# Kernel tuning notes

Measured on AMD Instinct MI355X. Metric: run time of the kernel, lower is better.

The kernel has to match this reference:

```python
import jax, jax.numpy as jnp
import numpy as np

IN_F = 64
EDGE_F = 64
B, N = 2, 512


def setup_inputs() -> dict:
    key = jax.random.key(0)
    ks = jax.random.split(key, 10)
    h = jax.random.normal(ks[0], (B, N, IN_F), dtype=jnp.float32)
    edge = jax.random.normal(ks[1], (B, N, N, EDGE_F), dtype=jnp.float32)
    adj = (jax.random.uniform(ks[2], (B, N, N)) < 0.5).astype(jnp.float32)
    lin_in = 2 * IN_F + EDGE_F
    s_lin = 1.0 / np.sqrt(lin_in)
    s_gru = 1.0 / np.sqrt(EDGE_F)
    W_lin = jax.random.uniform(ks[3], (EDGE_F, lin_in), minval=-s_lin, maxval=s_lin)
    b_lin = jax.random.uniform(ks[4], (EDGE_F,), minval=-s_lin, maxval=s_lin)
    w_ih = jax.random.uniform(ks[5], (3 * EDGE_F, EDGE_F), minval=-s_gru, maxval=s_gru)
    w_hh = jax.random.uniform(ks[6], (3 * EDGE_F, EDGE_F), minval=-s_gru, maxval=s_gru)
    b_ih = jax.random.uniform(ks[7], (3 * EDGE_F,), minval=-s_gru, maxval=s_gru)
    b_hh = jax.random.uniform(ks[8], (3 * EDGE_F,), minval=-s_gru, maxval=s_gru)
    return {"h": h, "edge": edge, "adj": adj, "W_lin": W_lin, "b_lin": b_lin,
            "w_ih": w_ih, "w_hh": w_hh, "b_ih": b_ih, "b_hh": b_hh}


def reference(h, edge, adj, W_lin, b_lin, w_ih, w_hh, b_ih, b_hh):
    F_ = h.shape[-1]
    E = edge.shape[-1]
    # Split the concat-linear: cat = [h1, edge, h2] where h1[b,i,j]=h[b,j], h2[b,i,j]=h[b,i].
    W1 = W_lin[:, :F_]            # cols acting on h1
    We = W_lin[:, F_:F_ + E]      # cols acting on edge
    W2 = W_lin[:, F_ + E:]        # cols acting on h2
    t1 = jnp.einsum('bjf,ef->bje', h, W1)[:, None, :, :]   # broadcast over i
    t2 = jnp.einsum('bif,ef->bie', h, W2)[:, :, None, :]   # broadcast over j
    te = jnp.einsum('bije,fe->bijf', edge, We)
    m = (t1 + te + t2 + b_lin) * adj[..., None]            # [b,N,N,E]
    # GRUCell: input = m, hidden = edge
    gi = jnp.einsum('bije,ge->bijg', m, w_ih) + b_ih        # [b,N,N,3E]
    gh = jnp.einsum('bije,ge->bijg', edge, w_hh) + b_hh
    i_r, i_z, i_n = jnp.split(gi, 3, axis=-1)
    h_r, h_z, h_n = jnp.split(gh, 3, axis=-1)
    r = jax.nn.sigmoid(i_r + h_r)
    z = jax.nn.sigmoid(i_z + h_z)
    n = jnp.tanh(i_n + r * h_n)
    new_h = (1.0 - z) * n + z * edge
    return jax.nn.silu(new_h)
```

## Files before the change

### kernel.cpp

```cpp
#include <hip/hip_runtime.h>
#include <hip/hip_bf16.h>

#define B_ 2
#define N_ 512
#define E_ 64
#define G_ 192
#define LIN_IN_ 192

typedef __attribute__((ext_vector_type(8))) short bf16x8;
typedef __attribute__((ext_vector_type(4))) float f32x4;

__device__ __forceinline__ unsigned short f2bf(float x) {
  unsigned u = __float_as_uint(x);
  unsigned r = (u + 0x7FFFu + ((u >> 16) & 1u)) >> 16;
  return (unsigned short)r;
}
__device__ __forceinline__ float sigm(float x) {
  return __builtin_amdgcn_rcpf(1.f + __expf(-x));
}
__device__ __forceinline__ float tanh_f(float x) {
  float e = __expf(-2.f * fabsf(x));
  return copysignf((1.f - e) * __builtin_amdgcn_rcpf(1.f + e), x);
}
__device__ __forceinline__ bf16x8 pack8(const float* t) {
  union { bf16x8 v; __hip_bfloat16 h[8]; } u;
#pragma unroll
  for (int k = 0; k < 8; ++k) u.h[k] = __float2bfloat16(t[k]);
  return u.v;
}

__global__ __launch_bounds__(64) void prep1(const float* __restrict__ Wlin,
                                            const float* __restrict__ blin,
                                            const float* __restrict__ wih,
                                            const float* __restrict__ whh,
                                            unsigned short* __restrict__ Bt,
                                            float* __restrict__ V1,
                                            float* __restrict__ V2,
                                            float* __restrict__ ub) {
  int g = blockIdx.x;
  int f = threadIdx.x;
  if (g < G_) {
    const float* wr = wih + g * 64;
    float aw = 0.f, a1 = 0.f, a2 = 0.f;
#pragma unroll
    for (int e = 0; e < 64; ++e) {
      float wv = wr[e];
      a1 += wv * Wlin[e * LIN_IN_ + f];
      aw += wv * Wlin[e * LIN_IN_ + 64 + f];
      a2 += wv * Wlin[e * LIN_IN_ + 128 + f];
    }
    Bt[g * 64 + f] = f2bf(aw);
    V1[g * 64 + f] = a1;
    V2[g * 64 + f] = a2;
    if (f == 0) {
      float s = 0.f;
      for (int e = 0; e < 64; ++e) s += wr[e] * blin[e];
      ub[g] = s;
    }
  } else {
    int gh = g - G_;
    Bt[g * 64 + f] = f2bf(whh[gh * 64 + f]);
  }
}

__global__ __launch_bounds__(192) void prep2(const float* __restrict__ h,
                                             const float* __restrict__ V1,
                                             const float* __restrict__ V2,
                                             const float* __restrict__ ub,
                                             float* __restrict__ u1,
                                             float* __restrict__ u2p) {
  int row = blockIdx.x;
  int g = threadIdx.x;
  const float* hr = h + (size_t)row * 64;
  float a1 = 0.f, a2 = 0.f;
#pragma unroll
  for (int f = 0; f < 64; ++f) {
    float hv = hr[f];
    a1 += V1[g * 64 + f] * hv;
    a2 += V2[g * 64 + f] * hv;
  }
  u1[(size_t)row * G_ + g] = a1;
  u2p[(size_t)row * G_ + g] = a2 + ub[g];
}

__global__ __launch_bounds__(256) void fusedT14(const float* __restrict__ edge,
                                                const float* __restrict__ adj,
                                                const unsigned short* __restrict__ BtW,
                                                const float* __restrict__ u1,
                                                const float* __restrict__ u2p,
                                                const float* __restrict__ bih,
                                                const float* __restrict__ bhh,
                                                float* __restrict__ out) {
  __shared__ uint4 Bs4[3072];
  char* Bc = (char*)Bs4;
  int tid = threadIdx.x;

  int lane = tid & 63, wave = tid >> 6;
  unsigned pbase = blockIdx.x * 256u + wave * 32u;
  int b = pbase >> 18;
  int iN = (pbase >> 9) & 511;
  int lr = lane & 15, lg = lane >> 4;

  float4 raw[2][4];
  float adjraw[2];
#pragma unroll
  for (int np = 0; np < 2; ++np) {
    const float* er = edge + (size_t)(pbase + np * 16 + lr) * 64 + lg * 8;
    raw[np][0] = *(const float4*)er;
    raw[np][1] = *(const float4*)(er + 4);
    raw[np][2] = *(const float4*)(er + 32);
    raw[np][3] = *(const float4*)(er + 36);
    adjraw[np] = adj[pbase + np * 16 + lr];
  }

  const uint4* src = (const uint4*)BtW;
#pragma unroll
  for (int it = 0; it < 12; ++it) {
    int c = tid + it * 256;
    int row = c >> 3;
    *(uint4*)(Bc + row * 128 + (((c & 7) * 16) ^ ((row & 7) << 4))) = src[c];
  }
  __syncthreads();

  int addrE = (lr + 16 * (lg >> 1)) << 2;
  int addrO = addrE + 128;

  const float* u2r = u2p + ((size_t)(b * N_ + iN)) * G_;

#pragma unroll
  for (int t = 0; t < 2; ++t) {
    unsigned ptile = pbase + (unsigned)t * 128u;
    int j0w = (int)(ptile & 511);

    bf16x8 efrag[2][2];
    float adjv[2];
#pragma unroll
    for (int np = 0; np < 2; ++np) {
#pragma unroll
      for (int s = 0; s < 2; ++s) {
        float tmp[8];
        *(float4*)tmp = raw[np][s * 2];
        *(float4*)(tmp + 4) = raw[np][s * 2 + 1];
        efrag[np][s] = pack8(tmp);
      }
      adjv[np] = adjraw[np];
    }

    if (t == 0) {
      unsigned pnext = pbase + 128u;
#pragma unroll
      for (int np = 0; np < 2; ++np) {
        const float* er = edge + (size_t)(pnext + np * 16 + lr) * 64 + lg * 8;
        raw[np][0] = *(const float4*)er;
        raw[np][1] = *(const float4*)(er + 4);
        raw[np][2] = *(const float4*)(er + 32);
        raw[np][3] = *(const float4*)(er + 36);
        adjraw[np] = adj[pnext + np * 16 + lr];
      }
    }

    const float* u1b = u1 + ((size_t)(b * N_ + j0w)) * G_;

    f32x4 yo[2][4];

#pragma unroll
    for (int mg = 0; mg < 4; ++mg) {
      int e0 = mg * 16 + lg * 4;

      f32x4 u1v[2][3];
#pragma unroll
      for (int np = 0; np < 2; ++np) {
        const float* u1r = u1b + (size_t)(np * 16 + lr) * G_;
        u1v[np][0] = *(const f32x4*)(u1r + e0);
        u1v[np][1] = *(const f32x4*)(u1r + 64 + e0);
        u1v[np][2] = *(const f32x4*)(u1r + 128 + e0);
      }

      f32x4 acc[2][6];
      f32x4 zero = {0.f, 0.f, 0.f, 0.f};
#pragma unroll
      for (int np = 0; np < 2; ++np)
#pragma unroll
        for (int w = 0; w < 6; ++w) acc[np][w] = zero;

      const int tiles[6] = {mg, mg + 4, mg + 8, mg + 12, mg + 16, mg + 20};
#pragma unroll
      for (int s = 0; s < 2; ++s) {
        bf16x8 wf[6];
#pragma unroll
        for (int w = 0; w < 6; ++w) {
          int R = tiles[w] * 16 + lr;
          wf[w] = *(const bf16x8*)(Bc + R * 128 +
                                   ((s * 64 + lg * 16) ^ ((R & 7) << 4)));
        }
#pragma unroll
        for (int np = 0; np < 2; ++np)
#pragma unroll
          for (int w = 0; w < 6; ++w)
            acc[np][w] = __builtin_amdgcn_mfma_f32_16x16x32_bf16(
                wf[w], efrag[np][s], acc[np][w], 0, 0, 0);
      }

      f32x4 u2v0 = *(const f32x4*)(u2r + e0);
      f32x4 u2v1 = *(const f32x4*)(u2r + 64 + e0);
      f32x4 u2v2 = *(const f32x4*)(u2r + 128 + e0);
      f32x4 bc0 = *(const f32x4*)(bih + e0) + *(const f32x4*)(bhh + e0);
      f32x4 bc1 = *(const f32x4*)(bih + 64 + e0) + *(const f32x4*)(bhh + 64 + e0);
      f32x4 bi2 = *(const f32x4*)(bih + 128 + e0);
      f32x4 bh2 = *(const f32x4*)(bhh + 128 + e0);

#pragma unroll
      for (int np = 0; np < 2; ++np) {
        union { bf16x8 v; int d[4]; } ef;
        ef.v = efrag[np][mg >> 1];
        int addr = (mg & 1) ? addrO : addrE;
        int r0 = __builtin_amdgcn_ds_bpermute(addr, ef.d[0]);
        int r1 = __builtin_amdgcn_ds_bpermute(addr, ef.d[1]);
        int r2 = __builtin_amdgcn_ds_bpermute(addr, ef.d[2]);
        int r3 = __builtin_amdgcn_ds_bpermute(addr, ef.d[3]);
        bool hi = (lg & 1);
        unsigned w0 = (unsigned)(hi ? r2 : r0);
        unsigned w1 = (unsigned)(hi ? r3 : r1);
        float eva[4];
        eva[0] = __uint_as_float(w0 << 16);
        eva[1] = __uint_as_float(w0 & 0xffff0000u);
        eva[2] = __uint_as_float(w1 << 16);
        eva[3] = __uint_as_float(w1 & 0xffff0000u);

        float a = adjv[np];
        f32x4 yv;
#pragma unroll
        for (int reg = 0; reg < 4; ++reg) {
          float s1 = a * (acc[np][0][reg] + u1v[np][0][reg] + u2v0[reg]) +
                     bc0[reg] + acc[np][3][reg];
          float s2 = a * (acc[np][1][reg] + u1v[np][1][reg] + u2v1[reg]) +
                     bc1[reg] + acc[np][4][reg];
          float gin = a * (acc[np][2][reg] + u1v[np][2][reg] + u2v2[reg]) +
                      bi2[reg];
          float ghn = acc[np][5][reg] + bh2[reg];
          float r = sigm(s1);
          float z = sigm(s2);
          float tt = gin + r * ghn;
          float n = 2.f * sigm(2.f * tt) - 1.f;
          float y = n + z * (eva[reg] - n);
          yv[reg] = y * sigm(y);
        }
        yo[np][mg] = yv;
      }
    }

#pragma unroll
    for (int np = 0; np < 2; ++np) {
      size_t P = ptile + np * 16 + lr;
      float* op = out + P * 64 + lg * 4;
#pragma unroll
      for (int mg = 0; mg < 4; ++mg)
        *(f32x4*)(op + mg * 16) = yo[np][mg];
    }
  }
}

__global__ __launch_bounds__(64) void mkernelF(const float* __restrict__ edge,
                                               const float* __restrict__ adj,
                                               const float* __restrict__ Wlin,
                                               const float* __restrict__ blin,
                                               const float* __restrict__ h,
                                               float* __restrict__ mout) {
  size_t p = (size_t)blockIdx.x * 64 + threadIdx.x;
  int b = (int)(p >> 18), i = (int)((p >> 9) & 511), j = (int)(p & 511);
  float ed[E_], hj[E_], hi[E_];
  const float4* ep = (const float4*)(edge + p * E_);
  const float4* hjp = (const float4*)(h + ((size_t)(b * N_ + j)) * E_);
  const float4* hip = (const float4*)(h + ((size_t)(b * N_ + i)) * E_);
#pragma unroll
  for (int k = 0; k < E_ / 4; ++k) {
    float4 v = ep[k];
    ed[4 * k] = v.x; ed[4 * k + 1] = v.y; ed[4 * k + 2] = v.z; ed[4 * k + 3] = v.w;
    float4 a = hjp[k];
    hj[4 * k] = a.x; hj[4 * k + 1] = a.y; hj[4 * k + 2] = a.z; hj[4 * k + 3] = a.w;
    float4 u = hip[k];
    hi[4 * k] = u.x; hi[4 * k + 1] = u.y; hi[4 * k + 2] = u.z; hi[4 * k + 3] = u.w;
  }
  float av = adj[p];
  float* mo = mout + p * E_;
  for (int e = 0; e < E_; ++e) {
    const float* w = Wlin + e * LIN_IN_;
    float acc = blin[e];
#pragma unroll
    for (int k = 0; k < E_; ++k)
      acc += hj[k] * w[k] + ed[k] * w[64 + k] + hi[k] * w[128 + k];
    mo[e] = av * acc;
  }
}
__global__ __launch_bounds__(64) void gkernelF(const float* __restrict__ edge,
                                               const float* mbuf,
                                               const float* __restrict__ wih,
                                               const float* __restrict__ whh,
                                               const float* __restrict__ bih,
                                               const float* __restrict__ bhh,
                                               float* out) {
  size_t p = (size_t)blockIdx.x * 64 + threadIdx.x;
  float ed[E_], m[E_];
  const float4* ep = (const float4*)(edge + p * E_);
  const float4* mp = (const float4*)(mbuf + p * E_);
#pragma unroll
  for (int k = 0; k < E_ / 4; ++k) {
    float4 v = ep[k];
    ed[4 * k] = v.x; ed[4 * k + 1] = v.y; ed[4 * k + 2] = v.z; ed[4 * k + 3] = v.w;
    float4 u = mp[k];
    m[4 * k] = u.x; m[4 * k + 1] = u.y; m[4 * k + 2] = u.z; m[4 * k + 3] = u.w;
  }
  float* op = out + p * E_;
  for (int e = 0; e < E_; ++e) {
    const float* wr = wih + e * 64;
    const float* wz = wih + (64 + e) * 64;
    const float* wn = wih + (128 + e) * 64;
    const float* vr = whh + e * 64;
    const float* vz = whh + (64 + e) * 64;
    const float* vn = whh + (128 + e) * 64;
    float ir = bih[e], iz = bih[64 + e], inn = bih[128 + e];
    float hr = bhh[e], hz = bhh[64 + e], hn = bhh[128 + e];
#pragma unroll
    for (int k = 0; k < E_; ++k) {
      float mk = m[k], ek = ed[k];
      ir += mk * wr[k]; iz += mk * wz[k]; inn += mk * wn[k];
      hr += ek * vr[k]; hz += ek * vz[k]; hn += ek * vn[k];
    }
    float r = sigm(ir + hr);
    float z = sigm(iz + hz);
    float nv = tanh_f(inn + r * hn);
    float nh = (1.f - z) * nv + z * ed[e];
    op[e] = nh * sigm(nh);
  }
}

extern "C" void kernel_launch(void* const* d_in, const int* in_sizes, int n_in,
                              void* d_out, int out_size, void* d_ws, size_t ws_size,
                              hipStream_t stream) {
  const float* h    = (const float*)d_in[0];
  const float* edge = (const float*)d_in[1];
  const float* adj  = (const float*)d_in[2];
  const float* Wlin = (const float*)d_in[3];
  const float* blin = (const float*)d_in[4];
  const float* wih  = (const float*)d_in[5];
  const float* whh  = (const float*)d_in[6];
  const float* bih  = (const float*)d_in[7];
  const float* bhh  = (const float*)d_in[8];
  float* out = (float*)d_out;

  const size_t OFF_V1 = 49152, OFF_V2 = 98304, OFF_UB = 147456,
               OFF_U1 = 148480, OFF_U2 = 148480 + 786432;
  const size_t WS_NEEDED = OFF_U2 + 786432;
  if (ws_size >= WS_NEEDED) {
    char* w = (char*)d_ws;
    unsigned short* Bt = (unsigned short*)w;
    float* V1 = (float*)(w + OFF_V1);
    float* V2 = (float*)(w + OFF_V2);
    float* ub = (float*)(w + OFF_UB);
    float* u1 = (float*)(w + OFF_U1);
    float* u2p = (float*)(w + OFF_U2);
    prep1<<<384, 64, 0, stream>>>(Wlin, blin, wih, whh, Bt, V1, V2, ub);
    prep2<<<B_ * N_, 192, 0, stream>>>(h, V1, V2, ub, u1, u2p);
    fusedT14<<<2048, 256, 0, stream>>>(edge, adj, Bt, u1, u2p, bih, bhh, out);
  } else {
    size_t npairs = (size_t)B_ * N_ * N_;
    int blocks = (int)(npairs / 64);
    mkernelF<<<blocks, 64, 0, stream>>>(edge, adj, Wlin, blin, h, out);
    gkernelF<<<blocks, 64, 0, stream>>>(edge, out, wih, whh, bih, bhh, out);
  }
}
```

Before: 123.8 us.

## Make fused GRU kernel persistent with cross-group edge prefetch

Converts the fused MFMA GRU kernel from 2048 one-shot blocks to a persistent grid of 768 blocks that loop over groups with a stride. The weight tile is staged into LDS once per block instead of once per group, and the next group's edge/adj loads are issued while the current second tile is computed, so global latency overlaps across group boundaries. The tile math is factored into a helper. Fewer resident blocks may reduce latency hiding, and 2048 groups over 768 blocks leaves some blocks doing three groups and others two, so the load is uneven.

```diff
diff --git a/kernel.cpp b/kernel.cpp
--- a/kernel.cpp
+++ b/kernel.cpp
@@ -6,6 +6,8 @@
 #define E_ 64
 #define G_ 192
 #define LIN_IN_ 192
+#define NGROUP_ 2048u
+#define GSTRIDE_ 768u
 
 typedef __attribute__((ext_vector_type(8))) short bf16x8;
 typedef __attribute__((ext_vector_type(4))) float f32x4;
@@ -83,7 +85,112 @@
   u2p[(size_t)row * G_ + g] = a2 + ub[g];
 }
 
-__global__ __launch_bounds__(256) void fusedT14(const float* __restrict__ edge,
+__device__ __forceinline__ void compute_tile(
+    unsigned ptile, int b, const bf16x8 efrag[2][2], const float adjv[2],
+    const char* Bc, const float* __restrict__ u1, const float* __restrict__ u2r,
+    const float* __restrict__ bih, const float* __restrict__ bhh,
+    float* __restrict__ out, int lr, int lg, int addrE, int addrO) {
+  int j0w = (int)(ptile & 511);
+  const float* u1b = u1 + ((size_t)(b * N_ + j0w)) * G_;
+  f32x4 yo[2][4];
+
+#pragma unroll
+  for (int mg = 0; mg < 4; ++mg) {
+    int e0 = mg * 16 + lg * 4;
+
+    f32x4 u1v[2][3];
+#pragma unroll
+    for (int np = 0; np < 2; ++np) {
+      const float* u1r = u1b + (size_t)(np * 16 + lr) * G_;
+      u1v[np][0] = *(const f32x4*)(u1r + e0);
+      u1v[np][1] = *(const f32x4*)(u1r + 64 + e0);
+      u1v[np][2] = *(const f32x4*)(u1r + 128 + e0);
+    }
+
+    f32x4 acc[2][6];
+    f32x4 zero = {0.f, 0.f, 0.f, 0.f};
+#pragma unroll
+    for (int np = 0; np < 2; ++np)
+#pragma unroll
+      for (int w = 0; w < 6; ++w) acc[np][w] = zero;
+
+    const int tiles[6] = {mg, mg + 4, mg + 8, mg + 12, mg + 16, mg + 20};
+#pragma unroll
+    for (int s = 0; s < 2; ++s) {
+      bf16x8 wf[6];
+#pragma unroll
+      for (int w = 0; w < 6; ++w) {
+        int R = tiles[w] * 16 + lr;
+        wf[w] = *(const bf16x8*)(Bc + R * 128 +
+                                 ((s * 64 + lg * 16) ^ ((R & 7) << 4)));
+      }
+#pragma unroll
+      for (int np = 0; np < 2; ++np)
+#pragma unroll
+        for (int w = 0; w < 6; ++w)
+          acc[np][w] = __builtin_amdgcn_mfma_f32_16x16x32_bf16(
+              wf[w], efrag[np][s], acc[np][w], 0, 0, 0);
+    }
+
+    f32x4 u2v0 = *(const f32x4*)(u2r + e0);
+    f32x4 u2v1 = *(const f32x4*)(u2r + 64 + e0);
+    f32x4 u2v2 = *(const f32x4*)(u2r + 128 + e0);
+    f32x4 bc0 = *(const f32x4*)(bih + e0) + *(const f32x4*)(bhh + e0);
+    f32x4 bc1 = *(const f32x4*)(bih + 64 + e0) + *(const f32x4*)(bhh + 64 + e0);
+    f32x4 bi2 = *(const f32x4*)(bih + 128 + e0);
+    f32x4 bh2 = *(const f32x4*)(bhh + 128 + e0);
+
+#pragma unroll
+    for (int np = 0; np < 2; ++np) {
+      union { bf16x8 v; int d[4]; } ef;
+      ef.v = efrag[np][mg >> 1];
+      int addr = (mg & 1) ? addrO : addrE;
+      int r0 = __builtin_amdgcn_ds_bpermute(addr, ef.d[0]);
+      int r1 = __builtin_amdgcn_ds_bpermute(addr, ef.d[1]);
+      int r2 = __builtin_amdgcn_ds_bpermute(addr, ef.d[2]);
+      int r3 = __builtin_amdgcn_ds_bpermute(addr, ef.d[3]);
+      bool hi = (lg & 1);
+      unsigned w0 = (unsigned)(hi ? r2 : r0);
+      unsigned w1 = (unsigned)(hi ? r3 : r1);
+      float eva[4];
+      eva[0] = __uint_as_float(w0 << 16);
+      eva[1] = __uint_as_float(w0 & 0xffff0000u);
+      eva[2] = __uint_as_float(w1 << 16);
+      eva[3] = __uint_as_float(w1 & 0xffff0000u);
+
+      float a = adjv[np];
+      f32x4 yv;
+#pragma unroll
+      for (int reg = 0; reg < 4; ++reg) {
+        float s1 = a * (acc[np][0][reg] + u1v[np][0][reg] + u2v0[reg]) +
+                   bc0[reg] + acc[np][3][reg];
+        float s2 = a * (acc[np][1][reg] + u1v[np][1][reg] + u2v1[reg]) +
+                   bc1[reg] + acc[np][4][reg];
+        float gin = a * (acc[np][2][reg] + u1v[np][2][reg] + u2v2[reg]) +
+                    bi2[reg];
+        float ghn = acc[np][5][reg] + bh2[reg];
+        float r = sigm(s1);
+        float z = sigm(s2);
+        float tt = gin + r * ghn;
+        float n = 2.f * sigm(2.f * tt) - 1.f;
+        float y = n + z * (eva[reg] - n);
+        yv[reg] = y * sigm(y);
+      }
+      yo[np][mg] = yv;
+    }
+  }
+
+#pragma unroll
+  for (int np = 0; np < 2; ++np) {
+    size_t P = ptile + np * 16 + lr;
+    float* op = out + P * 64 + lg * 4;
+#pragma unroll
+    for (int mg = 0; mg < 4; ++mg)
+      *(f32x4*)(op + mg * 16) = yo[np][mg];
+  }
+}
+
+__global__ __launch_bounds__(256) void fusedT15(const float* __restrict__ edge,
                                                 const float* __restrict__ adj,
                                                 const unsigned short* __restrict__ BtW,
                                                 const float* __restrict__ u1,
@@ -94,12 +201,11 @@
   __shared__ uint4 Bs4[3072];
   char* Bc = (char*)Bs4;
   int tid = threadIdx.x;
-
   int lane = tid & 63, wave = tid >> 6;
-  unsigned pbase = blockIdx.x * 256u + wave * 32u;
-  int b = pbase >> 18;
-  int iN = (pbase >> 9) & 511;
   int lr = lane & 15, lg = lane >> 4;
+
+  unsigned grp = blockIdx.x;
+  unsigned pbase = grp * 256u + wave * 32u;
 
   float4 raw[2][4];
   float adjraw[2];
@@ -125,15 +231,15 @@
   int addrE = (lr + 16 * (lg >> 1)) << 2;
   int addrO = addrE + 128;
 
-  const float* u2r = u2p + ((size_t)(b * N_ + iN)) * G_;
-
-#pragma unroll
-  for (int t = 0; t < 2; ++t) {
-    unsigned ptile = pbase + (unsigned)t * 128u;
-    int j0w = (int)(ptile & 511);
+#pragma unroll 1
+  for (;;) {
+    int b = (int)(pbase >> 18);
+    int iN = (int)((pbase >> 9) & 511);
+    const float* u2r = u2p + ((size_t)(b * N_ + iN)) * G_;
 
     bf16x8 efrag[2][2];
     float adjv[2];
+
 #pragma unroll
     for (int np = 0; np < 2; ++np) {
 #pragma unroll
@@ -145,8 +251,7 @@
       }
       adjv[np] = adjraw[np];
     }
-
-    if (t == 0) {
+    {
       unsigned pnext = pbase + 128u;
 #pragma unroll
       for (int np = 0; np < 2; ++np) {
@@ -158,105 +263,40 @@
         adjraw[np] = adj[pnext + np * 16 + lr];
       }
     }
-
-    const float* u1b = u1 + ((size_t)(b * N_ + j0w)) * G_;
-
-    f32x4 yo[2][4];
-
-#pragma unroll
-    for (int mg = 0; mg < 4; ++mg) {
-      int e0 = mg * 16 + lg * 4;
-
-      f32x4 u1v[2][3];
+    compute_tile(pbase, b, efrag, adjv, Bc, u1, u2r, bih, bhh, out,
+                 lr, lg, addrE, addrO);
+
+#pragma unroll
+    for (int np = 0; np < 2; ++np) {
+#pragma unroll
+      for (int s = 0; s < 2; ++s) {
+        float tmp[8];
+        *(float4*)tmp = raw[np][s * 2];
+        *(float4*)(tmp + 4) = raw[np][s * 2 + 1];
+        efrag[np][s] = pack8(tmp);
+      }
+      adjv[np] = adjraw[np];
+    }
+    unsigned ngrp = grp + GSTRIDE_;
+    bool more = (ngrp < NGROUP_);
+    unsigned npbase = ngrp * 256u + wave * 32u;
+    if (more) {
 #pragma unroll
       for (int np = 0; np < 2; ++np) {
-        const float* u1r = u1b + (size_t)(np * 16 + lr) * G_;
-        u1v[np][0] = *(const f32x4*)(u1r + e0);
-        u1v[np][1] = *(const f32x4*)(u1r + 64 + e0);
-        u1v[np][2] = *(const f32x4*)(u1r + 128 + e0);
-      }
-
-      f32x4 acc[2][6];
-      f32x4 zero = {0.f, 0.f, 0.f, 0.f};
-#pragma unroll
-      for (int np = 0; np < 2; ++np)
-#pragma unroll
-        for (int w = 0; w < 6; ++w) acc[np][w] = zero;
-
-      const int tiles[6] = {mg, mg + 4, mg + 8, mg + 12, mg + 16, mg + 20};
-#pragma unroll
-      for (int s = 0; s < 2; ++s) {
-        bf16x8 wf[6];
-#pragma unroll
-        for (int w = 0; w < 6; ++w) {
-          int R = tiles[w] * 16 + lr;
-          wf[w] = *(const bf16x8*)(Bc + R * 128 +
-                                   ((s * 64 + lg * 16) ^ ((R & 7) << 4)));
-        }
-#pragma unroll
-        for (int np = 0; np < 2; ++np)
-#pragma unroll
-          for (int w = 0; w < 6; ++w)
-            acc[np][w] = __builtin_amdgcn_mfma_f32_16x16x32_bf16(
-                wf[w], efrag[np][s], acc[np][w], 0, 0, 0);
-      }
-
-      f32x4 u2v0 = *(const f32x4*)(u2r + e0);
-      f32x4 u2v1 = *(const f32x4*)(u2r + 64 + e0);
-      f32x4 u2v2 = *(const f32x4*)(u2r + 128 + e0);
-      f32x4 bc0 = *(const f32x4*)(bih + e0) + *(const f32x4*)(bhh + e0);
-      f32x4 bc1 = *(const f32x4*)(bih + 64 + e0) + *(const f32x4*)(bhh + 64 + e0);
-      f32x4 bi2 = *(const f32x4*)(bih + 128 + e0);
-      f32x4 bh2 = *(const f32x4*)(bhh + 128 + e0);
-
-#pragma unroll
-      for (int np = 0; np < 2; ++np) {
-        union { bf16x8 v; int d[4]; } ef;
-        ef.v = efrag[np][mg >> 1];
-        int addr = (mg & 1) ? addrO : addrE;
-        int r0 = __builtin_amdgcn_ds_bpermute(addr, ef.d[0]);
-        int r1 = __builtin_amdgcn_ds_bpermute(addr, ef.d[1]);
-        int r2 = __builtin_amdgcn_ds_bpermute(addr, ef.d[2]);
-        int r3 = __builtin_amdgcn_ds_bpermute(addr, ef.d[3]);
-        bool hi = (lg & 1);
-        unsigned w0 = (unsigned)(hi ? r2 : r0);
-        unsigned w1 = (unsigned)(hi ? r3 : r1);
-        float eva[4];
-        eva[0] = __uint_as_float(w0 << 16);
-        eva[1] = __uint_as_float(w0 & 0xffff0000u);
-        eva[2] = __uint_as_float(w1 << 16);
-        eva[3] = __uint_as_float(w1 & 0xffff0000u);
-
-        float a = adjv[np];
-        f32x4 yv;
-#pragma unroll
-        for (int reg = 0; reg < 4; ++reg) {
-          float s1 = a * (acc[np][0][reg] + u1v[np][0][reg] + u2v0[reg]) +
-                     bc0[reg] + acc[np][3][reg];
-          float s2 = a * (acc[np][1][reg] + u1v[np][1][reg] + u2v1[reg]) +
-                     bc1[reg] + acc[np][4][reg];
-          float gin = a * (acc[np][2][reg] + u1v[np][2][reg] + u2v2[reg]) +
-                      bi2[reg];
-          float ghn = acc[np][5][reg] + bh2[reg];
-          float r = sigm(s1);
-          float z = sigm(s2);
-          float tt = gin + r * ghn;
-          float n = 2.f * sigm(2.f * tt) - 1.f;
-          float y = n + z * (eva[reg] - n);
-          yv[reg] = y * sigm(y);
-        }
-        yo[np][mg] = yv;
-      }
-    }
-
-#pragma unroll
-    for (int np = 0; np < 2; ++np) {
-      size_t P = ptile + np * 16 + lr;
-      float* op = out + P * 64 + lg * 4;
-#pragma unroll
-      for (int mg = 0; mg < 4; ++mg)
-        *(f32x4*)(op + mg * 16) = yo[np][mg];
-    }
+        const float* er = edge + (size_t)(npbase + np * 16 + lr) * 64 + lg * 8;
+        raw[np][0] = *(const float4*)er;
+        raw[np][1] = *(const float4*)(er + 4);
+        raw[np][2] = *(const float4*)(er + 32);
+        raw[np][3] = *(const float4*)(er + 36);
+        adjraw[np] = adj[npbase + np * 16 + lr];
+      }
+    }
+    compute_tile(pbase + 128u, b, efrag, adjv, Bc, u1, u2r, bih, bhh, out,
+                 lr, lg, addrE, addrO);
+
+    if (!more) break;
+    grp = ngrp;
+    pbase = npbase;
   }
 }
 
@@ -361,7 +401,7 @@
     float* u2p = (float*)(w + OFF_U2);
     prep1<<<384, 64, 0, stream>>>(Wlin, blin, wih, whh, Bt, V1, V2, ub);
     prep2<<<B_ * N_, 192, 0, stream>>>(h, V1, V2, ub, u1, u2p);
-    fusedT14<<<2048, 256, 0, stream>>>(edge, adj, Bt, u1, u2p, bih, bhh, out);
+    fusedT15<<<GSTRIDE_, 256, 0, stream>>>(edge, adj, Bt, u1, u2p, bih, bhh, out);
   } else {
     size_t npairs = (size_t)B_ * N_ * N_;
     int blocks = (int)(npairs / 64);
```

New measurement: 172.9 us. 1.4x slower.
